# Kernel tuning notes

Measured on AMD Instinct MI355X. Metric: run time of the kernel, lower is better.

The kernel has to match this reference:

```python
import jax, jax.numpy as jnp
import numpy as np

# DeepSeek V4 MLA sparse attention dims
T = 512            # query tokens
H = 64             # attention heads (SUPPORTED_HEAD_COUNTS)
KV_LORA = 512      # kv_lora_rank (value dim = latent nope part)
ROPE = 64          # qk_rope_head_dim
D = KV_LORA + ROPE # 576 = head_dim (matches alignment=576 in cache spec)
N_KV = 8192        # cached compressed-KV tokens
TOPK = 1024        # top-k selected tokens per query
SCALE = 1.0 / np.sqrt(D).astype(np.float32)


def setup_inputs() -> dict:
    key = jax.random.key(0)
    k1, k2, k3, k4 = jax.random.split(key, 4)
    q = jax.random.normal(k1, (T, H, D), dtype=jnp.float32)
    kv = jax.random.normal(k2, (N_KV, D), dtype=jnp.float32)   # compressed KV latent cache (1 kv head)
    topk_idx = jax.random.randint(k3, (T, TOPK), 0, N_KV, dtype=jnp.int32)
    sink = jax.random.normal(k4, (H,), dtype=jnp.float32)       # per-head attention sink logit
    return {"q": q, "kv": kv, "topk_idx": topk_idx, "sink": sink}


def reference(q, kv, topk_idx, sink):
    # Sparse MLA: each query token attends only to its top-k latent cache slots.
    valid = topk_idx >= 0                       # invalid slots marked negative
    idx = jnp.maximum(topk_idx, 0)
    g = kv[idx]                                  # [T, K, D] gathered latents
    # scores over gathered subset: [T, H, K]
    scores = jnp.einsum('thd,tkd->thk', q, g) * SCALE
    scores = jnp.where(valid[:, None, :], scores, -jnp.inf)
    # sink-aware softmax: sink acts as an extra logit with zero value
    m = jnp.maximum(jnp.max(scores, axis=-1), sink[None, :])   # [T, H]
    p = jnp.exp(scores - m[..., None])                          # [T, H, K]
    denom = jnp.sum(p, axis=-1) + jnp.exp(sink[None, :] - m)    # [T, H]
    # value = nope part (first KV_LORA dims) of latent -> output [T, H, KV_LORA]
    out = jnp.einsum('thk,tkv->thv', p, g[..., :KV_LORA]) / denom[..., None]
    return out
```

## Files before the change

kernel.cpp:

```cpp
#include <hip/hip_runtime.h>
#include <hip/hip_bf16.h>

#define T_TOK 512
#define NH    64
#define HD    576
#define DVAL  512
#define NKV   8192
#define TOPK  1024
#define KT    32
#define NITER (TOPK / KT)
#define KSTEPS (HD / 32)
#define SCALE 0.041666666666666664f

typedef __attribute__((ext_vector_type(4))) float f32x4;
typedef __attribute__((ext_vector_type(8))) _Float16 half8;
typedef __attribute__((ext_vector_type(4))) unsigned short us4;
typedef __attribute__((ext_vector_type(8))) unsigned short us8;
typedef __attribute__((ext_vector_type(4))) int i32x4;

__device__ __forceinline__ unsigned short f2h(float x) {
    _Float16 h = (_Float16)x;
    return __builtin_bit_cast(unsigned short, h);
}

__global__ void cvt_kv_f16(const float* __restrict__ kv, unsigned short* __restrict__ kvb) {
    int i = blockIdx.x * 256 + threadIdx.x;
    const f32x4* src = (const f32x4*)kv + (size_t)i * 2;
    f32x4 a = src[0];
    f32x4 b = src[1];
    us8 w;
    w[0]=f2h(a[0]); w[1]=f2h(a[1]); w[2]=f2h(a[2]); w[3]=f2h(a[3]);
    w[4]=f2h(b[0]); w[5]=f2h(b[1]); w[6]=f2h(b[2]); w[7]=f2h(b[3]);
    ((us8*)kvb)[i] = w;
}

#define G_LD  584
#define P_LD  40
#define GT_IDX(row,key) (((((row) << 5) | (key))) ^ ((((row) >> 2) & 7) << 3))

__device__ __forceinline__ void stage_load(
    const unsigned short* __restrict__ kvb, const int* __restrict__ tkrow,
    int it, int w8, int lm, int kg, us4* v, us4* vrope)
{
    const int* ip = tkrow + it * KT + kg * 8;
    i32x4 ra = *(const i32x4*)ip;
    i32x4 rb = *(const i32x4*)(ip + 4);
    int rows[8];
    rows[0]=ra[0]; rows[1]=ra[1]; rows[2]=ra[2]; rows[3]=ra[3];
    rows[4]=rb[0]; rows[5]=rb[1]; rows[6]=rb[2]; rows[7]=rb[3];
    int d0 = w8 * 64 + lm * 4;
    #pragma unroll
    for (int j = 0; j < 8; j++) {
        int r = rows[j] < 0 ? 0 : rows[j];
        v[j] = *(const us4*)(kvb + (size_t)r * HD + d0);
    }
    int kr = tkrow[it * KT + w8 * 4 + kg];
    if (kr < 0) kr = 0;
    *vrope = *(const us4*)(kvb + (size_t)kr * HD + 512 + lm * 4);
}

__device__ __forceinline__ void stage_write(
    int w8, int lm, int kg, const us4* v, us4 vrope,
    unsigned short (*gp)[G_LD], unsigned short* gtp)
{
    int d0 = w8 * 64 + lm * 4;
    #pragma unroll
    for (int j = 0; j < 8; j++)
        *(us4*)&gp[kg * 8 + j][d0] = v[j];
    #pragma unroll
    for (int dd = 0; dd < 4; dd++) {
        us8 wv;
        wv[0]=v[0][dd]; wv[1]=v[1][dd]; wv[2]=v[2][dd]; wv[3]=v[3][dd];
        wv[4]=v[4][dd]; wv[5]=v[5][dd]; wv[6]=v[6][dd]; wv[7]=v[7][dd];
        *(us8*)&gtp[GT_IDX(d0 + dd, kg * 8)] = wv;
    }
    *(us4*)&gp[w8 * 4 + kg][512 + lm * 4] = vrope;
}

__global__ __launch_bounds__(768, 3) void mla_sparse_kernel(
    const float* __restrict__ q, const int* __restrict__ topk,
    const float* __restrict__ sink, const unsigned short* __restrict__ kvb,
    float* __restrict__ out)
{
    __shared__ unsigned short g2[2][KT][G_LD];
    __shared__ unsigned short gtb[2][DVAL * 32];
    __shared__ unsigned short pbuf[2][NH][P_LD];
    __shared__ float arun[2][NH];
    __shared__ float lrunL[NH];

    const int t    = blockIdx.x;
    const int tid  = threadIdx.x;
    const int lane = tid & 63;
    const int quad = lane >> 4;
    const int l16  = lane & 15;
    const int wave = __builtin_amdgcn_readfirstlane(tid >> 6);
    const int* tkrow = topk + (size_t)t * TOPK;

    if (wave < 4) {
        const int w = wave;
        half8 qf[KSTEPS];
        {
            const float* qrow = q + ((size_t)t * NH + (w * 16 + l16)) * HD;
            #pragma unroll
            for (int ks = 0; ks < KSTEPS; ks++) {
                int d0 = ks * 32 + quad * 8;
                f32x4 a = *(const f32x4*)(qrow + d0);
                f32x4 b = *(const f32x4*)(qrow + d0 + 4);
                half8 h;
                h[0]=(_Float16)a[0]; h[1]=(_Float16)a[1]; h[2]=(_Float16)a[2]; h[3]=(_Float16)a[3];
                h[4]=(_Float16)b[0]; h[5]=(_Float16)b[1]; h[6]=(_Float16)b[2]; h[7]=(_Float16)b[3];
                qf[ks] = h;
            }
        }
        f32x4 sk = *(const f32x4*)(sink + w * 16 + quad * 4);
        float m_run[4], l_run[4];
        #pragma unroll
        for (int r = 0; r < 4; r++) { m_run[r] = sk[r]; l_run[r] = 1.0f; }

        __syncthreads();

        for (int k = 0; k <= NITER; k++) {
            if (k < NITER) {
                const int par = k & 1;
                f32x4 s0 = {0.f,0.f,0.f,0.f}, s1 = {0.f,0.f,0.f,0.f};
                #pragma unroll
                for (int ks = 0; ks < KSTEPS; ks++) {
                    half8 b0 = *(const half8*)&g2[par][l16][ks * 32 + quad * 8];
                    half8 b1 = *(const half8*)&g2[par][16 + l16][ks * 32 + quad * 8];
                    s0 = __builtin_amdgcn_mfma_f32_16x16x32_f16(qf[ks], b0, s0, 0, 0, 0);
                    s1 = __builtin_amdgcn_mfma_f32_16x16x32_f16(qf[ks], b1, s1, 0, 0, 0);
                }
                int i0 = tkrow[k * KT + l16];
                int i1 = tkrow[k * KT + 16 + l16];
                float bb0 = i0 < 0 ? -__builtin_inff() : 0.0f;
                float bb1 = i1 < 0 ? -__builtin_inff() : 0.0f;
                float v0[4], v1[4], tmx[4];
                #pragma unroll
                for (int r = 0; r < 4; r++) {
                    v0[r] = s0[r] * SCALE + bb0;
                    v1[r] = s1[r] * SCALE + bb1;
                    tmx[r] = fmaxf(v0[r], v1[r]);
                }
                #pragma unroll
                for (int m = 1; m < 16; m <<= 1) {
                    #pragma unroll
                    for (int r = 0; r < 4; r++)
                        tmx[r] = fmaxf(tmx[r], __shfl_xor(tmx[r], m));
                }
                float p0[4], p1[4], ps[4], al[4];
                #pragma unroll
                for (int r = 0; r < 4; r++) {
                    float mn = fmaxf(m_run[r], tmx[r]);
                    al[r] = __expf(m_run[r] - mn);
                    p0[r] = __expf(v0[r] - mn);
                    p1[r] = __expf(v1[r] - mn);
                    ps[r] = p0[r] + p1[r];
                    m_run[r] = mn;
                }
                #pragma unroll
                for (int m = 1; m < 16; m <<= 1) {
                    #pragma unroll
                    for (int r = 0; r < 4; r++)
                        ps[r] += __shfl_xor(ps[r], m);
                }
                #pragma unroll
                for (int r = 0; r < 4; r++)
                    l_run[r] = l_run[r] * al[r] + ps[r];
                const int hb = w * 16 + quad * 4;
                if (l16 == 0) {
                    f32x4 a4; a4[0]=al[0]; a4[1]=al[1]; a4[2]=al[2]; a4[3]=al[3];
                    *(f32x4*)&arun[par][hb] = a4;
                }
                #pragma unroll
                for (int r = 0; r < 4; r++) {
                    pbuf[par][hb + r][l16]      = f2h(p0[r]);
                    pbuf[par][hb + r][16 + l16] = f2h(p1[r]);
                }
            }
            __syncthreads();
        }
        if (l16 == 0) {
            f32x4 l4; l4[0]=l_run[0]; l4[1]=l_run[1]; l4[2]=l_run[2]; l4[3]=l_run[3];
            *(f32x4*)&lrunL[w * 16 + quad * 4] = l4;
        }
        __syncthreads();
    } else {
        const int w8   = wave - 4;
        const int col0 = w8 * 64;
        const int kg   = quad;
        const int lm   = l16;
        f32x4 acc[4][4];
        f32x4 zero = {0.f,0.f,0.f,0.f};
        #pragma unroll
        for (int mt = 0; mt < 4; mt++)
            #pragma unroll
            for (int nt = 0; nt < 4; nt++) acc[mt][nt] = zero;

        {
            us4 v[8]; us4 vrope;
            stage_load(kvb, tkrow, 0, w8, lm, kg, v, &vrope);
            stage_write(w8, lm, kg, v, vrope, g2[0], gtb[0]);
        }
        __syncthreads();

        for (int k = 0; k <= NITER; k++) {
            if (k == 0) {
                us4 v[8]; us4 vrope;
                stage_load(kvb, tkrow, 1, w8, lm, kg, v, &vrope);
                stage_write(w8, lm, kg, v, vrope, g2[1], gtb[1]);
            } else {
                const int par = (k - 1) & 1;
                half8 pa[4], vb[4];
                #pragma unroll
                for (int mt = 0; mt < 4; mt++)
                    pa[mt] = *(const half8*)&pbuf[par][mt * 16 + l16][quad * 8];
                #pragma unroll
                for (int nt = 0; nt < 4; nt++)
                    vb[nt] = *(const half8*)&gtb[par][GT_IDX(col0 + nt * 16 + l16, quad * 8)];
                asm volatile("s_waitcnt lgkmcnt(0)" ::: "memory");

                const bool do_stage = (k + 1) < NITER;
                us4 v[8]; us4 vrope;
                if (do_stage)
                    stage_load(kvb, tkrow, k + 1, w8, lm, kg, v, &vrope);

                #pragma unroll
                for (int mt = 0; mt < 4; mt++) {
                    f32x4 av = *(const f32x4*)&arun[par][mt * 16 + quad * 4];
                    #pragma unroll
                    for (int nt = 0; nt < 4; nt++) {
                        acc[mt][nt] *= av;
                        acc[mt][nt] = __builtin_amdgcn_mfma_f32_16x16x32_f16(pa[mt], vb[nt], acc[mt][nt], 0, 0, 0);
                    }
                }
                if (do_stage) {
                    const int spar = (k + 1) & 1;
                    stage_write(w8, lm, kg, v, vrope, g2[spar], gtb[spar]);
                }
            }
            __syncthreads();
        }
        __syncthreads();

        #pragma unroll
        for (int mt = 0; mt < 4; mt++) {
            f32x4 lv = *(const f32x4*)&lrunL[mt * 16 + quad * 4];
            f32x4 li;
            li[0] = 1.0f / lv[0]; li[1] = 1.0f / lv[1];
            li[2] = 1.0f / lv[2]; li[3] = 1.0f / lv[3];
            #pragma unroll
            for (int nt = 0; nt < 4; nt++) {
                int vcol = col0 + nt * 16 + l16;
                f32x4 r = acc[mt][nt] * li;
                #pragma unroll
                for (int rr = 0; rr < 4; rr++) {
                    int head = mt * 16 + quad * 4 + rr;
                    out[((size_t)t * NH + head) * DVAL + vcol] = r[rr];
                }
            }
        }
    }
}

extern "C" void kernel_launch(void* const* d_in, const int* in_sizes, int n_in,
                              void* d_out, int out_size, void* d_ws, size_t ws_size,
                              hipStream_t stream) {
    const float* q    = (const float*)d_in[0];
    const float* kv   = (const float*)d_in[1];
    const int*   topk = (const int*)d_in[2];
    const float* sink = (const float*)d_in[3];
    float* out = (float*)d_out;
    unsigned short* kvb = (unsigned short*)d_ws;

    cvt_kv_f16<<<NKV * HD / (256 * 8), 256, 0, stream>>>(kv, kvb);
    mla_sparse_kernel<<<T_TOK, 768, 0, stream>>>(q, topk, sink, kvb, out);
}
```

Before: 296.3 us.

## Deepen KV gather pipeline, fold scale into Q, use exp2 and DPP reductions

The producer waves now prefetch the gathered KV tile two iterations ahead using two register sets, and issue wider 8-element loads, so global-load latency overlaps more of the PV MFMA work. The softmax folds SCALE*log2e into Q, uses exp2, replaces shuffle reductions with DPP row ops, precomputes invalid-index bitmasks, splits the QK accumulators for more MFMA ILP, and skips the rescale when every alpha is 1. Barriers become raw s_barrier with lgkmcnt waits, and setprio raises MFMA priority. These add register pressure and rely on subtle barrier and LDS ordering, which could introduce hazards.

Measured after the change: 272.2 us. 1.09x faster.

```diff
diff --git a/kernel.cpp b/kernel.cpp
--- a/kernel.cpp
+++ b/kernel.cpp
@@ -11,6 +11,8 @@
 #define NITER (TOPK / KT)
 #define KSTEPS (HD / 32)
 #define SCALE 0.041666666666666664f
+#define LOG2E 1.4426950408889634f
+#define QSCL  (SCALE * LOG2E)
 
 typedef __attribute__((ext_vector_type(4))) float f32x4;
 typedef __attribute__((ext_vector_type(8))) _Float16 half8;
@@ -22,6 +24,40 @@
     _Float16 h = (_Float16)x;
     return __builtin_bit_cast(unsigned short, h);
 }
+
+__device__ __forceinline__ float fexp2(float x) {
+#if __has_builtin(__builtin_amdgcn_exp2f)
+    return __builtin_amdgcn_exp2f(x);
+#else
+    return __expf(x * 0.6931471805599453f);
+#endif
+}
+
+template<int CTRL>
+__device__ __forceinline__ float dppmv(float x) {
+    int r = __builtin_amdgcn_update_dpp(0, __builtin_bit_cast(int, x), CTRL, 0xF, 0xF, true);
+    return __builtin_bit_cast(float, r);
+}
+__device__ __forceinline__ float red16max(float x) {
+    x = fmaxf(x, dppmv<0xB1>(x));
+    x = fmaxf(x, dppmv<0x4E>(x));
+    x = fmaxf(x, dppmv<0x141>(x));
+    x = fmaxf(x, dppmv<0x140>(x));
+    return x;
+}
+__device__ __forceinline__ float red16sum(float x) {
+    x += dppmv<0xB1>(x);
+    x += dppmv<0x4E>(x);
+    x += dppmv<0x141>(x);
+    x += dppmv<0x140>(x);
+    return x;
+}
+
+#define TICK_BARRIER() do {                                   \
+    asm volatile("s_waitcnt lgkmcnt(0)" ::: "memory");        \
+    __builtin_amdgcn_s_barrier();                             \
+    asm volatile("" ::: "memory");                            \
+} while (0)
 
 __global__ void cvt_kv_f16(const float* __restrict__ kv, unsigned short* __restrict__ kvb) {
     int i = blockIdx.x * 256 + threadIdx.x;
@@ -38,43 +74,86 @@
 #define P_LD  40
 #define GT_IDX(row,key) (((((row) << 5) | (key))) ^ ((((row) >> 2) & 7) << 3))
 
+struct StageRegs { us8 v[4]; us4 rope; };
+
 __device__ __forceinline__ void stage_load(
     const unsigned short* __restrict__ kvb, const int* __restrict__ tkrow,
-    int it, int w8, int lm, int kg, us4* v, us4* vrope)
+    int it, int w8, int kg, int lm, int quad, int l16, StageRegs& R)
 {
-    const int* ip = tkrow + it * KT + kg * 8;
-    i32x4 ra = *(const i32x4*)ip;
-    i32x4 rb = *(const i32x4*)(ip + 4);
-    int rows[8];
-    rows[0]=ra[0]; rows[1]=ra[1]; rows[2]=ra[2]; rows[3]=ra[3];
-    rows[4]=rb[0]; rows[5]=rb[1]; rows[6]=rb[2]; rows[7]=rb[3];
-    int d0 = w8 * 64 + lm * 4;
-    #pragma unroll
-    for (int j = 0; j < 8; j++) {
-        int r = rows[j] < 0 ? 0 : rows[j];
-        v[j] = *(const us4*)(kvb + (size_t)r * HD + d0);
-    }
-    int kr = tkrow[it * KT + w8 * 4 + kg];
+    const int* ip = tkrow + it * KT + kg * 4;
+    i32x4 r4 = *(const i32x4*)ip;
+    int d0 = w8 * 64 + lm * 8;
+    #pragma unroll
+    for (int j = 0; j < 4; j++) {
+        int r = r4[j] < 0 ? 0 : r4[j];
+        R.v[j] = *(const us8*)(kvb + (size_t)r * HD + d0);
+    }
+    int kr = tkrow[it * KT + w8 * 4 + quad];
     if (kr < 0) kr = 0;
-    *vrope = *(const us4*)(kvb + (size_t)kr * HD + 512 + lm * 4);
+    R.rope = *(const us4*)(kvb + (size_t)kr * HD + 512 + l16 * 4);
 }
 
 __device__ __forceinline__ void stage_write(
-    int w8, int lm, int kg, const us4* v, us4 vrope,
+    int w8, int kg, int lm, int quad, int l16, const StageRegs& R,
     unsigned short (*gp)[G_LD], unsigned short* gtp)
 {
-    int d0 = w8 * 64 + lm * 4;
-    #pragma unroll
-    for (int j = 0; j < 8; j++)
-        *(us4*)&gp[kg * 8 + j][d0] = v[j];
-    #pragma unroll
-    for (int dd = 0; dd < 4; dd++) {
-        us8 wv;
-        wv[0]=v[0][dd]; wv[1]=v[1][dd]; wv[2]=v[2][dd]; wv[3]=v[3][dd];
-        wv[4]=v[4][dd]; wv[5]=v[5][dd]; wv[6]=v[6][dd]; wv[7]=v[7][dd];
-        *(us8*)&gtp[GT_IDX(d0 + dd, kg * 8)] = wv;
-    }
-    *(us4*)&gp[w8 * 4 + kg][512 + lm * 4] = vrope;
+    int d0 = w8 * 64 + lm * 8;
+    #pragma unroll
+    for (int j = 0; j < 4; j++)
+        *(us8*)&gp[kg * 4 + j][d0] = R.v[j];
+    #pragma unroll
+    for (int e = 0; e < 8; e++) {
+        us4 wv;
+        wv[0] = R.v[0][e]; wv[1] = R.v[1][e]; wv[2] = R.v[2][e]; wv[3] = R.v[3][e];
+        *(us4*)&gtp[GT_IDX(d0 + e, kg * 4)] = wv;
+    }
+    *(us4*)&gp[w8 * 4 + quad][512 + l16 * 4] = R.rope;
+}
+
+__device__ __forceinline__ void pv_tick(
+    int tau, const unsigned short* __restrict__ kvb, const int* __restrict__ tkrow,
+    int w8, int kg, int lm, int quad, int l16, int col0,
+    StageRegs& Lset, StageRegs& Wset,
+    unsigned short (*g2p)[G_LD], unsigned short* gtp,
+    unsigned short (*pb)[P_LD], const float* ar,
+    f32x4 (&acc)[4][4])
+{
+    if (tau + 2 < NITER)
+        stage_load(kvb, tkrow, tau + 2, w8, kg, lm, quad, l16, Lset);
+
+    f32x4 avv[4];
+    bool one = true;
+    #pragma unroll
+    for (int mt = 0; mt < 4; mt++) {
+        avv[mt] = *(const f32x4*)&ar[mt * 16 + quad * 4];
+        one = one && (avv[mt][0] == 1.f) && (avv[mt][1] == 1.f)
+                  && (avv[mt][2] == 1.f) && (avv[mt][3] == 1.f);
+    }
+    if (!__all((int)one)) {
+        #pragma unroll
+        for (int mt = 0; mt < 4; mt++)
+            #pragma unroll
+            for (int nt = 0; nt < 4; nt++) acc[mt][nt] *= avv[mt];
+    }
+
+    half8 pa[4];
+    #pragma unroll
+    for (int mt = 0; mt < 4; mt++)
+        pa[mt] = *(const half8*)&pb[mt * 16 + l16][quad * 8];
+
+    __builtin_amdgcn_s_setprio(1);
+    #pragma unroll
+    for (int nt = 0; nt < 4; nt++) {
+        half8 vb = *(const half8*)&gtp[GT_IDX(col0 + nt * 16 + l16, quad * 8)];
+        #pragma unroll
+        for (int mt = 0; mt < 4; mt++)
+            acc[mt][nt] = __builtin_amdgcn_mfma_f32_16x16x32_f16(pa[mt], vb, acc[mt][nt], 0, 0, 0);
+    }
+    __builtin_amdgcn_s_setprio(0);
+
+    asm volatile("s_waitcnt lgkmcnt(0)" ::: "memory");
+    if (tau + 1 < NITER)
+        stage_write(w8, kg, lm, quad, l16, Wset, g2p, gtp);
 }
 
 __global__ __launch_bounds__(768, 3) void mla_sparse_kernel(
@@ -97,75 +176,79 @@
     const int* tkrow = topk + (size_t)t * TOPK;
 
     if (wave < 4) {
-        const int w = wave;
+        const int w  = wave;
+        const int qo = quad * 8;
         half8 qf[KSTEPS];
         {
             const float* qrow = q + ((size_t)t * NH + (w * 16 + l16)) * HD;
             #pragma unroll
             for (int ks = 0; ks < KSTEPS; ks++) {
-                int d0 = ks * 32 + quad * 8;
+                int d0 = ks * 32 + qo;
                 f32x4 a = *(const f32x4*)(qrow + d0);
                 f32x4 b = *(const f32x4*)(qrow + d0 + 4);
                 half8 h;
-                h[0]=(_Float16)a[0]; h[1]=(_Float16)a[1]; h[2]=(_Float16)a[2]; h[3]=(_Float16)a[3];
-                h[4]=(_Float16)b[0]; h[5]=(_Float16)b[1]; h[6]=(_Float16)b[2]; h[7]=(_Float16)b[3];
+                h[0]=(_Float16)(a[0]*QSCL); h[1]=(_Float16)(a[1]*QSCL);
+                h[2]=(_Float16)(a[2]*QSCL); h[3]=(_Float16)(a[3]*QSCL);
+                h[4]=(_Float16)(b[0]*QSCL); h[5]=(_Float16)(b[1]*QSCL);
+                h[6]=(_Float16)(b[2]*QSCL); h[7]=(_Float16)(b[3]*QSCL);
                 qf[ks] = h;
             }
         }
+        unsigned mb0 = 0, mb1 = 0;
+        #pragma unroll 4
+        for (int kk = 0; kk < NITER; kk++) {
+            mb0 |= (tkrow[kk * KT + l16]      < 0) ? (1u << kk) : 0u;
+            mb1 |= (tkrow[kk * KT + 16 + l16] < 0) ? (1u << kk) : 0u;
+        }
         f32x4 sk = *(const f32x4*)(sink + w * 16 + quad * 4);
         float m_run[4], l_run[4];
         #pragma unroll
-        for (int r = 0; r < 4; r++) { m_run[r] = sk[r]; l_run[r] = 1.0f; }
+        for (int r = 0; r < 4; r++) { m_run[r] = sk[r] * LOG2E; l_run[r] = 1.0f; }
 
         __syncthreads();
 
         for (int k = 0; k <= NITER; k++) {
             if (k < NITER) {
                 const int par = k & 1;
-                f32x4 s0 = {0.f,0.f,0.f,0.f}, s1 = {0.f,0.f,0.f,0.f};
-                #pragma unroll
-                for (int ks = 0; ks < KSTEPS; ks++) {
-                    half8 b0 = *(const half8*)&g2[par][l16][ks * 32 + quad * 8];
-                    half8 b1 = *(const half8*)&g2[par][16 + l16][ks * 32 + quad * 8];
-                    s0 = __builtin_amdgcn_mfma_f32_16x16x32_f16(qf[ks], b0, s0, 0, 0, 0);
-                    s1 = __builtin_amdgcn_mfma_f32_16x16x32_f16(qf[ks], b1, s1, 0, 0, 0);
-                }
-                int i0 = tkrow[k * KT + l16];
-                int i1 = tkrow[k * KT + 16 + l16];
-                float bb0 = i0 < 0 ? -__builtin_inff() : 0.0f;
-                float bb1 = i1 < 0 ? -__builtin_inff() : 0.0f;
+                const unsigned short (*gp)[G_LD] = g2[par];
+                f32x4 zero = {0.f,0.f,0.f,0.f};
+                f32x4 s0a = zero, s0b = zero, s1a = zero, s1b = zero;
+                __builtin_amdgcn_s_setprio(1);
+                #pragma unroll
+                for (int ks = 0; ks < KSTEPS; ks += 2) {
+                    half8 b0 = *(const half8*)&gp[l16][ks * 32 + qo];
+                    half8 b1 = *(const half8*)&gp[16 + l16][ks * 32 + qo];
+                    s0a = __builtin_amdgcn_mfma_f32_16x16x32_f16(qf[ks], b0, s0a, 0, 0, 0);
+                    s1a = __builtin_amdgcn_mfma_f32_16x16x32_f16(qf[ks], b1, s1a, 0, 0, 0);
+                    half8 c0 = *(const half8*)&gp[l16][ks * 32 + 32 + qo];
+                    half8 c1 = *(const half8*)&gp[16 + l16][ks * 32 + 32 + qo];
+                    s0b = __builtin_amdgcn_mfma_f32_16x16x32_f16(qf[ks+1], c0, s0b, 0, 0, 0);
+                    s1b = __builtin_amdgcn_mfma_f32_16x16x32_f16(qf[ks+1], c1, s1b, 0, 0, 0);
+                }
+                __builtin_amdgcn_s_setprio(0);
+                f32x4 s0 = s0a + s0b, s1 = s1a + s1b;
+
+                const float NEG = -__builtin_inff();
+                const bool bad0 = (mb0 >> k) & 1;
+                const bool bad1 = (mb1 >> k) & 1;
                 float v0[4], v1[4], tmx[4];
                 #pragma unroll
                 for (int r = 0; r < 4; r++) {
-                    v0[r] = s0[r] * SCALE + bb0;
-                    v1[r] = s1[r] * SCALE + bb1;
-                    tmx[r] = fmaxf(v0[r], v1[r]);
-                }
-                #pragma unroll
-                for (int m = 1; m < 16; m <<= 1) {
-                    #pragma unroll
-                    for (int r = 0; r < 4; r++)
-                        tmx[r] = fmaxf(tmx[r], __shfl_xor(tmx[r], m));
-                }
-                float p0[4], p1[4], ps[4], al[4];
+                    v0[r] = bad0 ? NEG : s0[r];
+                    v1[r] = bad1 ? NEG : s1[r];
+                    tmx[r] = red16max(fmaxf(v0[r], v1[r]));
+                }
+                float al[4], p0[4], p1[4];
                 #pragma unroll
                 for (int r = 0; r < 4; r++) {
                     float mn = fmaxf(m_run[r], tmx[r]);
-                    al[r] = __expf(m_run[r] - mn);
-                    p0[r] = __expf(v0[r] - mn);
-                    p1[r] = __expf(v1[r] - mn);
-                    ps[r] = p0[r] + p1[r];
+                    al[r] = fexp2(m_run[r] - mn);
+                    p0[r] = fexp2(v0[r] - mn);
+                    p1[r] = fexp2(v1[r] - mn);
                     m_run[r] = mn;
-                }
-                #pragma unroll
-                for (int m = 1; m < 16; m <<= 1) {
-                    #pragma unroll
-                    for (int r = 0; r < 4; r++)
-                        ps[r] += __shfl_xor(ps[r], m);
-                }
-                #pragma unroll
-                for (int r = 0; r < 4; r++)
-                    l_run[r] = l_run[r] * al[r] + ps[r];
+                    float ps = red16sum(p0[r] + p1[r]);
+                    l_run[r] = l_run[r] * al[r] + ps;
+                }
                 const int hb = w * 16 + quad * 4;
                 if (l16 == 0) {
                     f32x4 a4; a4[0]=al[0]; a4[1]=al[1]; a4[2]=al[2]; a4[3]=al[3];
@@ -177,7 +260,7 @@
                     pbuf[par][hb + r][16 + l16] = f2h(p1[r]);
                 }
             }
-            __syncthreads();
+            TICK_BARRIER();
         }
         if (l16 == 0) {
             f32x4 l4; l4[0]=l_run[0]; l4[1]=l_run[1]; l4[2]=l_run[2]; l4[3]=l_run[3];
@@ -187,8 +270,8 @@
     } else {
         const int w8   = wave - 4;
         const int col0 = w8 * 64;
-        const int kg   = quad;
-        const int lm   = l16;
+        const int kg   = lane >> 3;
+        const int lm   = lane & 7;
         f32x4 acc[4][4];
         f32x4 zero = {0.f,0.f,0.f,0.f};
         #pragma unroll
@@ -196,49 +279,23 @@
             #pragma unroll
             for (int nt = 0; nt < 4; nt++) acc[mt][nt] = zero;
 
-        {
-            us4 v[8]; us4 vrope;
-            stage_load(kvb, tkrow, 0, w8, lm, kg, v, &vrope);
-            stage_write(w8, lm, kg, v, vrope, g2[0], gtb[0]);
-        }
+        StageRegs A, B;
+        stage_load(kvb, tkrow, 0, w8, kg, lm, quad, l16, A);
+        stage_write(w8, kg, lm, quad, l16, A, g2[0], gtb[0]);
+        stage_load(kvb, tkrow, 1, w8, kg, lm, quad, l16, B);
         __syncthreads();
 
-        for (int k = 0; k <= NITER; k++) {
-            if (k == 0) {
-                us4 v[8]; us4 vrope;
-                stage_load(kvb, tkrow, 1, w8, lm, kg, v, &vrope);
-                stage_write(w8, lm, kg, v, vrope, g2[1], gtb[1]);
-            } else {
-                const int par = (k - 1) & 1;
-                half8 pa[4], vb[4];
-                #pragma unroll
-                for (int mt = 0; mt < 4; mt++)
-                    pa[mt] = *(const half8*)&pbuf[par][mt * 16 + l16][quad * 8];
-                #pragma unroll
-                for (int nt = 0; nt < 4; nt++)
-                    vb[nt] = *(const half8*)&gtb[par][GT_IDX(col0 + nt * 16 + l16, quad * 8)];
-                asm volatile("s_waitcnt lgkmcnt(0)" ::: "memory");
-
-                const bool do_stage = (k + 1) < NITER;
-                us4 v[8]; us4 vrope;
-                if (do_stage)
-                    stage_load(kvb, tkrow, k + 1, w8, lm, kg, v, &vrope);
-
-                #pragma unroll
-                for (int mt = 0; mt < 4; mt++) {
-                    f32x4 av = *(const f32x4*)&arun[par][mt * 16 + quad * 4];
-                    #pragma unroll
-                    for (int nt = 0; nt < 4; nt++) {
-                        acc[mt][nt] *= av;
-                        acc[mt][nt] = __builtin_amdgcn_mfma_f32_16x16x32_f16(pa[mt], vb[nt], acc[mt][nt], 0, 0, 0);
-                    }
-                }
-                if (do_stage) {
-                    const int spar = (k + 1) & 1;
-                    stage_write(w8, lm, kg, v, vrope, g2[spar], gtb[spar]);
-                }
-            }
-            __syncthreads();
+        stage_load(kvb, tkrow, 2, w8, kg, lm, quad, l16, A);
+        stage_write(w8, kg, lm, quad, l16, B, g2[1], gtb[1]);
+        TICK_BARRIER();
+
+        for (int k = 1; k < NITER; k += 2) {
+            pv_tick(k, kvb, tkrow, w8, kg, lm, quad, l16, col0,
+                    B, A, g2[0], gtb[0], pbuf[0], arun[0], acc);
+            TICK_BARRIER();
+            pv_tick(k + 1, kvb, tkrow, w8, kg, lm, quad, l16, col0,
+                    A, B, g2[1], gtb[1], pbuf[1], arun[1], acc);
+            TICK_BARRIER();
         }
         __syncthreads();
 
```
